# Kernel tuning notes

Measured on AMD Instinct MI355X. Metric: run time of the kernel, lower is better.

Reference implementation:

```python
import jax, jax.numpy as jnp
import numpy as np

H = 16        # num_attention_heads
KV = 4        # num_key_value_heads
HD = 128      # head_dim = hidden // H
N_REP = H // KV
ROPE_THETA = 10000.0


def _rope_cos_sin(T, dtype):
    inv_freq = 1.0 / (ROPE_THETA ** (jnp.arange(0, HD, 2, dtype=jnp.float32) / HD))
    pos = jnp.arange(T, dtype=jnp.float32)
    freqs = pos[:, None] * inv_freq[None, :]            # [T, HD/2]
    emb = jnp.concatenate([freqs, freqs], axis=-1)      # [T, HD]
    return jnp.cos(emb).astype(dtype), jnp.sin(emb).astype(dtype)


def _rotate_half(t):
    t1, t2 = jnp.split(t, 2, axis=-1)
    return jnp.concatenate([-t2, t1], axis=-1)


def setup_inputs() -> dict:
    key = jax.random.key(0)
    k1, k2, k3 = jax.random.split(key, 3)
    B, T, C = 2, 2048, 2048
    x = jax.random.normal(k1, (B, T, C), dtype=jnp.float32)
    attention_mask = jnp.ones((B, T), dtype=jnp.float32)
    w_qkv = jax.random.normal(k2, ((H + 2 * KV) * HD, C), dtype=jnp.float32) * 0.02
    w_proj = jax.random.normal(k3, (C, C), dtype=jnp.float32) * 0.02
    return {"x": x, "attention_mask": attention_mask, "w_qkv": w_qkv, "w_proj": w_proj}


def reference(x, attention_mask, w_qkv, w_proj):
    B, T, C = x.shape
    dtype = x.dtype
    neg = jnp.finfo(dtype).min

    # additive mask: causal (-big above diagonal) + padding ((1-mask)*min)
    i = jnp.arange(T)
    causal = jnp.where(i[None, :] <= i[:, None], 0.0, neg).astype(dtype)  # [T,T]
    add_mask = (1.0 - attention_mask)[:, None, None, :] * neg + causal[None, None]  # [B,1,T,T]

    # fused QKV projection
    qkv = jnp.einsum('btc,oc->bto', x, w_qkv)
    q = qkv[..., : H * HD].reshape(B, T, H, HD)
    k = qkv[..., H * HD : (H + KV) * HD].reshape(B, T, KV, HD)
    v = qkv[..., (H + KV) * HD :].reshape(B, T, KV, HD)

    # RoPE on q and k
    cos, sin = _rope_cos_sin(T, dtype)
    cos = cos[None, :, None, :]
    sin = sin[None, :, None, :]
    q = q * cos + _rotate_half(q) * sin
    k = k * cos + _rotate_half(k) * sin

    # GQA: repeat_interleave KV heads
    k = jnp.repeat(k, N_REP, axis=2)  # [B,T,H,HD]
    v = jnp.repeat(v, N_REP, axis=2)

    # [B,H,T,HD]
    q, k, v = (jnp.transpose(t, (0, 2, 1, 3)) for t in (q, k, v))

    scores = jnp.einsum('bhqd,bhkd->bhqk', q, k) * (1.0 / np.sqrt(HD))
    att = jax.nn.softmax(scores + add_mask, axis=-1)
    y = jnp.einsum('bhqk,bhkd->bhqd', att, v)
    y = jnp.transpose(y, (0, 2, 1, 3)).reshape(B, T, C)
    return jnp.einsum('btc,oc->bto', y, w_proj)
```

## Files before the change

kernel.cpp:

```cpp
#include <hip/hip_runtime.h>
#include <hip/hip_bf16.h>
#include <stdint.h>

typedef unsigned short u16;
typedef __attribute__((ext_vector_type(4))) float f32x4;
typedef __attribute__((ext_vector_type(16))) float f32x16;
typedef __attribute__((ext_vector_type(8))) __bf16 bf16x8;

#define NB 2
#define NT 2048
#define NC 2048
#define NH 16
#define NKV 4
#define HD 128
#define NQKV 3072
#define SCALE2 0.12751739f

__device__ __forceinline__ u16 f2bf(float f) {
  union { float f; uint32_t u; } c; c.f = f;
  uint32_t u = c.u + 0x7fffu + ((c.u >> 16) & 1u);
  return (u16)(u >> 16);
}
__device__ __forceinline__ float bf2f(u16 h) {
  union { uint32_t u; float f; } c; c.u = ((uint32_t)h) << 16;
  return c.f;
}
__device__ __forceinline__ uint32_t packbf2(float a, float b) {
  return (uint32_t)f2bf(a) | ((uint32_t)f2bf(b) << 16);
}

__device__ __forceinline__ void gload16(const void* g, void* lds) {
  __builtin_amdgcn_global_load_lds(
      (__attribute__((address_space(1))) void*)(uintptr_t)g,
      (__attribute__((address_space(3))) void*)(uint32_t)(uintptr_t)lds,
      16, 0, 0);
}

__global__ void cvt_bf16_kernel(const float* __restrict__ in, u16* __restrict__ out, int n4) {
  int stride = gridDim.x * blockDim.x;
  for (int i = blockIdx.x * blockDim.x + threadIdx.x; i < n4; i += stride) {
    float4 v = ((const float4*)in)[i];
    uint32_t lo = (uint32_t)f2bf(v.x) | ((uint32_t)f2bf(v.y) << 16);
    uint32_t hi = (uint32_t)f2bf(v.z) | ((uint32_t)f2bf(v.w) << 16);
    ((uint2*)out)[i] = make_uint2(lo, hi);
  }
}

__global__ void rope_tab_kernel(float* __restrict__ tab) {
  int idx = blockIdx.x * blockDim.x + threadIdx.x;
  int t = idx >> 6, i = idx & 63;
  float inv = expf(-(float)(2 * i) * (9.210340371976184f / 128.f));
  float f = (float)t * inv;
  tab[t * 128 + i] = cosf(f);
  tab[t * 128 + 64 + i] = sinf(f);
}

__global__ void rope_apply_kernel(const u16* __restrict__ qkv, const float* __restrict__ tab,
                                  u16* __restrict__ Q, u16* __restrict__ K) {
  int idx = blockIdx.x * blockDim.x + threadIdx.x;
  int i = idx & 63;
  int rest = idx >> 6;
  int hh = rest % 20;
  int bt = rest / 20;
  int t = bt & (NT - 1);
  int b = bt >> 11;
  const u16* src_row = qkv + (long)bt * NQKV;
  float c = tab[t * 128 + i], s = tab[t * 128 + 64 + i];
  if (hh < NH) {
    const u16* sp = src_row + hh * HD;
    float x0 = bf2f(sp[i]), x1 = bf2f(sp[i + 64]);
    u16* dp = Q + ((long)(b * NH + hh) * NT + t) * HD;
    dp[i] = f2bf((x0 * c - x1 * s) * SCALE2);
    dp[i + 64] = f2bf((x1 * c + x0 * s) * SCALE2);
  } else {
    int kh = hh - NH;
    const u16* sp = src_row + (NH + kh) * HD;
    float x0 = bf2f(sp[i]), x1 = bf2f(sp[i + 64]);
    u16* dp = K + ((long)(b * NKV + kh) * NT + t) * HD;
    dp[i] = f2bf(x0 * c - x1 * s);
    dp[i + 64] = f2bf(x1 * c + x0 * s);
  }
}

__global__ void vtrans_kernel(const u16* __restrict__ qkv, u16* __restrict__ Vt) {
  __shared__ u16 tile[64][72];
  const int t0 = (blockIdx.x >> 1) * 64;
  const int d0 = (blockIdx.x & 1) * 64;
  const int bkh = blockIdx.y;
  const int tid = threadIdx.x;
  const int tr = tid >> 2;
  const int tc = (tid & 3) * 16;
  const u16* src = qkv + ((long)((bkh >> 2) * NT) + t0 + tr) * NQKV +
                   (NH + NKV) * HD + (bkh & 3) * HD + d0 + tc;
  uint4 v0 = *(const uint4*)(src);
  uint4 v1 = *(const uint4*)(src + 8);
  *(uint4*)&tile[tr][tc] = v0;
  *(uint4*)&tile[tr][tc + 8] = v1;
  __syncthreads();
  const int dr = tid >> 2;
  const int tcc = (tid & 3) * 16;
  uint32_t pk[8];
#pragma unroll
  for (int e = 0; e < 8; ++e) {
    u16 a = tile[tcc + 2 * e][dr];
    u16 bq = tile[tcc + 2 * e + 1][dr];
    pk[e] = (uint32_t)a | ((uint32_t)bq << 16);
  }
  uint32_t tmp;
  tmp = pk[2]; pk[2] = pk[4]; pk[4] = tmp;
  tmp = pk[3]; pk[3] = pk[5]; pk[5] = tmp;
  const int d = d0 + dr;
  const int t = t0 + tcc;
  u16* dst = Vt + (long)bkh * HD * NT + (long)(d >> 1) * (2 * NT) +
             (t >> 6) * 128 + (d & 1) * 64 + (t & 48);
  *(uint4*)(dst) = *(uint4*)&pk[0];
  *(uint4*)(dst + 8) = *(uint4*)&pk[4];
}

template <int OUT_BF16, int NREP>
__global__ __launch_bounds__(512, 1) void gemm256_kernel(const u16* __restrict__ A,
                                                         const u16* __restrict__ Bm,
                                                         void* __restrict__ Cm,
                                                         int M, int N, int K) {
  constexpr int BN = NREP * 32;
  __shared__ __align__(16) u16 As[2][256 * 64];
  __shared__ __align__(16) u16 Bs[2][BN * 64];
  const int tid = threadIdx.x, lane = tid & 63, wid = tid >> 6;
  const int wr = wid >> 1, wc = wid & 1;
  const int g = lane >> 4, r = lane & 15;
  const long row0 = (long)blockIdx.y * 256;
  const long col0 = (long)blockIdx.x * BN;
  const int lrow = lane >> 3;
  const int lch = lane & 7;

  f32x4 acc[4][NREP] = {};

  auto stage = [&](int bufi, int kt) {
    const int k0 = kt * 64;
    u16* Ad = As[bufi];
    u16* Bd = Bs[bufi];
#pragma unroll
    for (int ii = 0; ii < 4; ++ii) {
      int rowl = wid * 32 + ii * 8 + lrow;
      const u16* src = A + (row0 + rowl) * (long)K + k0 + ((lch ^ (rowl & 7)) * 8);
      gload16(src, Ad + (wid * 32 + ii * 8) * 64);
    }
#pragma unroll
    for (int ii = 0; ii < NREP / 2; ++ii) {
      int rowl = wid * (NREP * 4) + ii * 8 + lrow;
      const u16* src = Bm + (col0 + rowl) * (long)K + k0 + ((lch ^ (rowl & 7)) * 8);
      gload16(src, Bd + (wid * (NREP * 4) + ii * 8) * 64);
    }
  };

  const int nt = K / 64;
  stage(0, 0);
  int buf = 0;
  for (int t = 0; t < nt; ++t) {
    if (t + 1 < nt) {
      stage(buf ^ 1, t + 1);
      __builtin_amdgcn_sched_barrier(0);
      if constexpr (NREP == 4) {
        asm volatile("s_waitcnt vmcnt(6)" ::: "memory");
      } else {
        asm volatile("s_waitcnt vmcnt(7)" ::: "memory");
      }
    } else {
      __builtin_amdgcn_sched_barrier(0);
      asm volatile("s_waitcnt vmcnt(0)" ::: "memory");
    }
    __builtin_amdgcn_sched_barrier(0);
    __builtin_amdgcn_s_barrier();
    __builtin_amdgcn_sched_barrier(0);

    const char* Ab = (const char*)As[buf];
    const char* Bb = (const char*)Bs[buf];
#pragma unroll
    for (int ks = 0; ks < 2; ++ks) {
      bf16x8 af[4], bfv[NREP];
#pragma unroll
      for (int mi = 0; mi < 4; ++mi) {
        int row = wr * 64 + mi * 16 + r;
        af[mi] = *(const bf16x8*)(Ab + row * 128 + (((4 * ks + g) ^ (row & 7)) * 16));
      }
#pragma unroll
      for (int ni = 0; ni < NREP; ++ni) {
        int row = wc * (NREP * 16) + ni * 16 + r;
        bfv[ni] = *(const bf16x8*)(Bb + row * 128 + (((4 * ks + g) ^ (row & 7)) * 16));
      }
      __builtin_amdgcn_s_setprio(1);
#pragma unroll
      for (int mi = 0; mi < 4; ++mi)
#pragma unroll
        for (int ni = 0; ni < NREP; ++ni)
          acc[mi][ni] = __builtin_amdgcn_mfma_f32_16x16x32_bf16(af[mi], bfv[ni], acc[mi][ni], 0, 0, 0);
      __builtin_amdgcn_s_setprio(0);
    }
    __builtin_amdgcn_sched_barrier(0);
    __builtin_amdgcn_s_barrier();
    __builtin_amdgcn_sched_barrier(0);
    buf ^= 1;
  }

#pragma unroll
  for (int mi = 0; mi < 4; ++mi)
#pragma unroll
    for (int ni = 0; ni < NREP; ++ni)
#pragma unroll
      for (int j = 0; j < 4; ++j) {
        long rr = row0 + wr * 64 + mi * 16 + g * 4 + j;
        long cc = col0 + wc * (NREP * 16) + ni * 16 + r;
        float v = acc[mi][ni][j];
        if (OUT_BF16) ((u16*)Cm)[rr * N + cc] = f2bf(v);
        else          ((float*)Cm)[rr * N + cc] = v;
      }
}

__global__ __launch_bounds__(256, 2) void attn_kernel(const u16* __restrict__ Qg,
                                                      const u16* __restrict__ Kg,
                                                      const u16* __restrict__ Vtg,
                                                      const float* __restrict__ amask,
                                                      u16* __restrict__ Y) {
  __shared__ __align__(16) u16 Ks[2][64 * 128];
  __shared__ __align__(16) u16 Vs[2][64 * 128];
  const int tid = threadIdx.x, lane = tid & 63, wid = tid >> 6;
  const int ql = lane & 31, hi = lane >> 5;
  const int id = blockIdx.x;
  const int h = id & 15;
  const int xp = (id >> 4) & 7;
  const int b = (id >> 7) & 1;
  const int half = id >> 8;
  const int qt = half ? 15 - xp : xp;
  const int q0 = qt * 128;
  const int kh = h >> 2;

  const u16* Kbh = Kg + (long)(b * NKV + kh) * NT * HD;
  const u16* Vtbh = Vtg + (long)(b * NKV + kh) * HD * NT;
  const u16* Qbh = Qg + (long)(b * NH + h) * NT * HD;
  const float* am_b = amask + b * NT;

  const int total = 2 * qt + 2;

  const int srow = lane >> 4;
  const int schunk = lane & 15;
  auto stageK = [&](u16* dst, int kv0) {
#pragma unroll
    for (int ii = 0; ii < 4; ++ii) {
      int kvl = wid * 16 + ii * 4 + srow;
      const u16* src = Kbh + (long)(kv0 + kvl) * HD + ((schunk ^ (kvl & 15)) * 8);
      gload16(src, dst + (wid * 16 + ii * 4) * 128);
    }
  };
  auto stageV = [&](u16* dst, int kv0) {
    const u16* vb = Vtbh + (kv0 >> 6) * 128;
#pragma unroll
    for (int ii = 0; ii < 4; ++ii) {
      int R = wid * 16 + ii * 4 + srow;
      const u16* src = vb + (long)R * (2 * NT) + ((schunk ^ (R & 15)) * 8);
      gload16(src, dst + (wid * 16 + ii * 4) * 128);
    }
  };

  bf16x8 qf[8];
  {
    const u16* Qrow = Qbh + (long)(q0 + wid * 32 + ql) * HD;
#pragma unroll
    for (int ks = 0; ks < 8; ++ks)
      qf[ks] = *(const bf16x8*)(Qrow + ks * 16 + 8 * hi);
  }

  stageK(Ks[0], 0);
  stageV(Vs[0], 0);
  __syncthreads();

  float m = -INFINITY;
  f32x4 lacc = {};
  f32x16 o[4] = {};
  int buf = 0;
  const int qi = q0 + wid * 32 + ql;

  for (int i = 0; i < total; ++i) {
    const int kv0 = i * 64;

    if (i + 1 < total) {
      stageK(Ks[buf ^ 1], (i + 1) * 64);
      stageV(Vs[buf ^ 1], (i + 1) * 64);
    }

    const char* Ksb = (const char*)Ks[buf];
    const char* Vsb = (const char*)Vs[buf];

    f32x16 s0a = {}, s0b = {}, s1a = {}, s1b = {};
    __builtin_amdgcn_s_setprio(1);
#pragma unroll
    for (int ks = 0; ks < 4; ++ks) {
      bf16x8 kf0 = *(const bf16x8*)(Ksb + ql * 256 + (((2 * ks + hi) ^ (ql & 15)) * 16));
      bf16x8 kf1 = *(const bf16x8*)(Ksb + (32 + ql) * 256 + (((2 * ks + hi) ^ (ql & 15)) * 16));
      s0a = __builtin_amdgcn_mfma_f32_32x32x16_bf16(kf0, qf[ks], s0a, 0, 0, 0);
      s1a = __builtin_amdgcn_mfma_f32_32x32x16_bf16(kf1, qf[ks], s1a, 0, 0, 0);
    }
#pragma unroll
    for (int ks = 4; ks < 8; ++ks) {
      bf16x8 kf0 = *(const bf16x8*)(Ksb + ql * 256 + (((2 * ks + hi) ^ (ql & 15)) * 16));
      bf16x8 kf1 = *(const bf16x8*)(Ksb + (32 + ql) * 256 + (((2 * ks + hi) ^ (ql & 15)) * 16));
      s0b = __builtin_amdgcn_mfma_f32_32x32x16_bf16(kf0, qf[ks], s0b, 0, 0, 0);
      s1b = __builtin_amdgcn_mfma_f32_32x32x16_bf16(kf1, qf[ks], s1b, 0, 0, 0);
    }
    __builtin_amdgcn_s_setprio(0);
    f32x16 s0 = s0a + s0b;
    f32x16 s1 = s1a + s1b;

    if (i >= 2 * qt) {
#pragma unroll
      for (int reg = 0; reg < 16; ++reg) {
        int kvl = (reg & 3) + 8 * (reg >> 2) + 4 * hi;
        if (kv0 + kvl > qi) s0[reg] = -INFINITY;
        if (kv0 + 32 + kvl > qi) s1[reg] = -INFINITY;
      }
    }

    float t16[16];
#pragma unroll
    for (int reg = 0; reg < 16; ++reg) t16[reg] = fmaxf(s0[reg], s1[reg]);
    float t8[8];
#pragma unroll
    for (int reg = 0; reg < 8; ++reg) t8[reg] = fmaxf(t16[reg], t16[reg + 8]);
    float t4[4];
#pragma unroll
    for (int reg = 0; reg < 4; ++reg) t4[reg] = fmaxf(t8[reg], t8[reg + 4]);
    float mxl = fmaxf(fmaxf(t4[0], t4[1]), fmaxf(t4[2], t4[3]));
    if (!__all(mxl <= m + 8.f)) {
      float mx = fmaxf(mxl, __shfl_xor(mxl, 32));
      float mnew = fmaxf(m, mx);
      float alpha = exp2f(m - mnew);
      m = mnew;
      lacc *= alpha;
#pragma unroll
      for (int dblk = 0; dblk < 4; ++dblk) o[dblk] *= alpha;
    }

    float4 am0[4], am1[4];
#pragma unroll
    for (int uu = 0; uu < 4; ++uu) {
      am0[uu] = *(const float4*)(am_b + kv0 + 8 * uu + 4 * hi);
      am1[uu] = *(const float4*)(am_b + kv0 + 32 + 8 * uu + 4 * hi);
    }
#pragma unroll
    for (int reg = 0; reg < 16; ++reg) {
      float p0 = exp2f(s0[reg] - m) * (&am0[reg >> 2].x)[reg & 3];
      float p1 = exp2f(s1[reg] - m) * (&am1[reg >> 2].x)[reg & 3];
      s0[reg] = p0; s1[reg] = p1;
      lacc[reg & 3] += p0 + p1;
    }

    bf16x8 pb[4];
#pragma unroll
    for (int ks = 0; ks < 4; ++ks) {
      union { __bf16 hh[8]; bf16x8 v; } pk;
      const int base = 8 * (ks & 1);
#pragma unroll
      for (int j = 0; j < 8; ++j)
        pk.hh[j] = (__bf16)((ks >= 2) ? s1[base + j] : s0[base + j]);
      pb[ks] = pk.v;
    }

    __builtin_amdgcn_s_setprio(1);
#pragma unroll
    for (int ks = 0; ks < 4; ++ks) {
#pragma unroll
      for (int dblk = 0; dblk < 4; ++dblk) {
        int drow = dblk * 16 + (ql >> 1);
        int gr = ((ql & 1) * 8 + 2 * ks + hi) ^ (drow & 15);
        bf16x8 va = *(const bf16x8*)(Vsb + drow * 256 + gr * 16);
        o[dblk] = __builtin_amdgcn_mfma_f32_32x32x16_bf16(va, pb[ks], o[dblk], 0, 0, 0);
      }
    }
    __builtin_amdgcn_s_setprio(0);

    __syncthreads();
    buf ^= 1;
  }

  {
    float l = (lacc[0] + lacc[1]) + (lacc[2] + lacc[3]);
    l += __shfl_xor(l, 32);
    float invl = 1.f / l;
    u16* Yrow = Y + ((long)b * NT + qi) * NC + h * HD;
#pragma unroll
    for (int dblk = 0; dblk < 4; ++dblk)
#pragma unroll
      for (int uu = 0; uu < 4; ++uu) {
        int d = dblk * 32 + 8 * uu + 4 * hi;
        int r0 = 4 * uu;
        *(uint2*)(Yrow + d) = make_uint2(
            packbf2(o[dblk][r0] * invl, o[dblk][r0 + 1] * invl),
            packbf2(o[dblk][r0 + 2] * invl, o[dblk][r0 + 3] * invl));
      }
  }
}

extern "C" void kernel_launch(void* const* d_in, const int* in_sizes, int n_in,
                              void* d_out, int out_size, void* d_ws, size_t ws_size,
                              hipStream_t stream) {
  const float* x = (const float*)d_in[0];
  const float* amask = (const float*)d_in[1];
  const float* w_qkv = (const float*)d_in[2];
  const float* w_proj = (const float*)d_in[3];

  const long MT = (long)NB * NT;
  char* ws = (char*)d_ws;
  size_t off = 0;
  auto carve = [&](size_t bytes) -> char* {
    char* p = ws + off;
    off += (bytes + 255) & ~(size_t)255;
    return p;
  };
  u16* xb   = (u16*)carve((size_t)MT * NC * 2);
  u16* wqb  = (u16*)carve((size_t)NQKV * NC * 2);
  u16* wpb  = (u16*)carve((size_t)NC * NC * 2);
  u16* qkvb = (u16*)carve((size_t)MT * NQKV * 2);
  float* tab = (float*)carve((size_t)NT * 128 * 4);

  u16* Qb = xb;
  u16* Kb = wqb;
  u16* Vtb = wqb + (size_t)NB * NKV * NT * HD;
  u16* Yb = qkvb;

  {
    int n4 = (int)(MT * NC / 4);
    cvt_bf16_kernel<<<dim3(2048), dim3(256), 0, stream>>>(x, xb, n4);
    n4 = (int)((long)NQKV * NC / 4);
    cvt_bf16_kernel<<<dim3(2048), dim3(256), 0, stream>>>(w_qkv, wqb, n4);
    n4 = (int)((long)NC * NC / 4);
    cvt_bf16_kernel<<<dim3(2048), dim3(256), 0, stream>>>(w_proj, wpb, n4);
  }
  rope_tab_kernel<<<dim3(NT * 64 / 256), dim3(256), 0, stream>>>(tab);
  gemm256_kernel<1, 6><<<dim3(NQKV / 192, MT / 256), dim3(512), 0, stream>>>(xb, wqb, qkvb, (int)MT, NQKV, NC);
  rope_apply_kernel<<<dim3(NB * NT * 20 * 64 / 256), dim3(256), 0, stream>>>(qkvb, tab, Qb, Kb);
  vtrans_kernel<<<dim3(NT / 64 * 2, NB * NKV), dim3(256), 0, stream>>>(qkvb, Vtb);
  attn_kernel<<<dim3(512), dim3(256), 0, stream>>>(Qb, Kb, Vtb, amask, Yb);
  gemm256_kernel<0, 4><<<dim3(NC / 128, MT / 256), dim3(512), 0, stream>>>(Yb, wpb, d_out, (int)MT, NC, NC);
}
```

Measured before the change: 199.0 us.

## Remap GEMM workgroups across XCDs and split A/B tile staging across k-substeps

The GEMM kernel now remaps its linear workgroup index so that consecutive tiles are spread across the eight XCDs. This is meant to improve L2 locality of shared A and B panels. The shared-memory load of each k-tile is also split: the A tile is prefetched at the start of the iteration and the B tile after the first k-substep, with a single vmcnt(4) wait. This spreads global loads more evenly across the MFMA work. The remap assumes the grid size is a multiple of eight, and the changed wait counts must stay consistent with the per-lane load counts.

```diff
diff --git a/kernel.cpp b/kernel.cpp
--- a/kernel.cpp
+++ b/kernel.cpp
@@ -128,23 +128,31 @@
   const int tid = threadIdx.x, lane = tid & 63, wid = tid >> 6;
   const int wr = wid >> 1, wc = wid & 1;
   const int g = lane >> 4, r = lane & 15;
-  const long row0 = (long)blockIdx.y * 256;
-  const long col0 = (long)blockIdx.x * BN;
+  int lin = blockIdx.y * gridDim.x + blockIdx.x;
+  const int nwg = gridDim.x * gridDim.y;
+  lin = (lin & 7) * (nwg >> 3) + (lin >> 3);
+  const int bx = lin % gridDim.x;
+  const int by = lin / gridDim.x;
+  const long row0 = (long)by * 256;
+  const long col0 = (long)bx * BN;
   const int lrow = lane >> 3;
   const int lch = lane & 7;
 
   f32x4 acc[4][NREP] = {};
 
-  auto stage = [&](int bufi, int kt) {
+  auto stageA = [&](int bufi, int kt) {
     const int k0 = kt * 64;
     u16* Ad = As[bufi];
-    u16* Bd = Bs[bufi];
 #pragma unroll
     for (int ii = 0; ii < 4; ++ii) {
       int rowl = wid * 32 + ii * 8 + lrow;
       const u16* src = A + (row0 + rowl) * (long)K + k0 + ((lch ^ (rowl & 7)) * 8);
       gload16(src, Ad + (wid * 32 + ii * 8) * 64);
     }
+  };
+  auto stageB = [&](int bufi, int kt) {
+    const int k0 = kt * 64;
+    u16* Bd = Bs[bufi];
 #pragma unroll
     for (int ii = 0; ii < NREP / 2; ++ii) {
       int rowl = wid * (NREP * 4) + ii * 8 + lrow;
@@ -154,17 +162,17 @@
   };
 
   const int nt = K / 64;
-  stage(0, 0);
+  stageA(0, 0);
+  stageB(0, 0);
   int buf = 0;
   for (int t = 0; t < nt; ++t) {
+    const char* Ab = (const char*)As[buf];
+    const char* Bb = (const char*)Bs[buf];
+
     if (t + 1 < nt) {
-      stage(buf ^ 1, t + 1);
+      stageA(buf ^ 1, t + 1);
       __builtin_amdgcn_sched_barrier(0);
-      if constexpr (NREP == 4) {
-        asm volatile("s_waitcnt vmcnt(6)" ::: "memory");
-      } else {
-        asm volatile("s_waitcnt vmcnt(7)" ::: "memory");
-      }
+      asm volatile("s_waitcnt vmcnt(4)" ::: "memory");
     } else {
       __builtin_amdgcn_sched_barrier(0);
       asm volatile("s_waitcnt vmcnt(0)" ::: "memory");
@@ -172,21 +180,43 @@
     __builtin_amdgcn_sched_barrier(0);
     __builtin_amdgcn_s_barrier();
     __builtin_amdgcn_sched_barrier(0);
-
-    const char* Ab = (const char*)As[buf];
-    const char* Bb = (const char*)Bs[buf];
-#pragma unroll
-    for (int ks = 0; ks < 2; ++ks) {
+    {
       bf16x8 af[4], bfv[NREP];
 #pragma unroll
       for (int mi = 0; mi < 4; ++mi) {
         int row = wr * 64 + mi * 16 + r;
-        af[mi] = *(const bf16x8*)(Ab + row * 128 + (((4 * ks + g) ^ (row & 7)) * 16));
+        af[mi] = *(const bf16x8*)(Ab + row * 128 + ((g ^ (row & 7)) * 16));
       }
 #pragma unroll
       for (int ni = 0; ni < NREP; ++ni) {
         int row = wc * (NREP * 16) + ni * 16 + r;
-        bfv[ni] = *(const bf16x8*)(Bb + row * 128 + (((4 * ks + g) ^ (row & 7)) * 16));
+        bfv[ni] = *(const bf16x8*)(Bb + row * 128 + ((g ^ (row & 7)) * 16));
+      }
+      __builtin_amdgcn_s_setprio(1);
+#pragma unroll
+      for (int mi = 0; mi < 4; ++mi)
+#pragma unroll
+        for (int ni = 0; ni < NREP; ++ni)
+          acc[mi][ni] = __builtin_amdgcn_mfma_f32_16x16x32_bf16(af[mi], bfv[ni], acc[mi][ni], 0, 0, 0);
+      __builtin_amdgcn_s_setprio(0);
+    }
+    __builtin_amdgcn_sched_barrier(0);
+    __builtin_amdgcn_s_barrier();
+    __builtin_amdgcn_sched_barrier(0);
+
+    if (t + 1 < nt) stageB(buf ^ 1, t + 1);
+    __builtin_amdgcn_sched_barrier(0);
+    {
+      bf16x8 af[4], bfv[NREP];
+#pragma unroll
+      for (int mi = 0; mi < 4; ++mi) {
+        int row = wr * 64 + mi * 16 + r;
+        af[mi] = *(const bf16x8*)(Ab + row * 128 + (((4 + g) ^ (row & 7)) * 16));
+      }
+#pragma unroll
+      for (int ni = 0; ni < NREP; ++ni) {
+        int row = wc * (NREP * 16) + ni * 16 + r;
+        bfv[ni] = *(const bf16x8*)(Bb + row * 128 + (((4 + g) ^ (row & 7)) * 16));
       }
       __builtin_amdgcn_s_setprio(1);
 #pragma unroll
```

After: 196.3 us. About the same (-1.3%).
